# Performance work log

Hardware: AMD Instinct MI355X
Metric: run time of the kernel (lower is better)

Reference implementation:

```python
import jax, jax.numpy as jnp
import numpy as np

B, S, D = 4, 1024, 384
NUM_ITEMS = 16384
NUM_CLUSTERS = 256
MAX_CLUSTER_SIZE = 128  # 16384/256 = 64 real members, padded to 128 with -1
NEG_INF = -1e9


def setup_inputs() -> dict:
    key = jax.random.key(0)
    k1, k2, k3, k4, k5 = jax.random.split(key, 5)
    hidden_states = jax.random.normal(k1, (B, S, D), dtype=jnp.float32)
    item_embeddings = jax.random.normal(k2, (NUM_ITEMS, D), dtype=jnp.float32) * 0.02
    cluster_embeddings = jax.random.normal(k3, (NUM_CLUSTERS, D), dtype=jnp.float32) * 0.02
    targets = jax.random.randint(k4, (B, S), 0, NUM_ITEMS, dtype=jnp.int32)
    item_mask = (jax.random.uniform(k5, (B, S)) < 0.8).astype(jnp.float32)
    # Deterministic round-robin clustering: item i -> cluster i % C, slot i // C
    cluster_assignments = (jnp.arange(NUM_ITEMS, dtype=jnp.int32) % NUM_CLUSTERS)
    ids = (jnp.arange(NUM_CLUSTERS, dtype=jnp.int32)[:, None]
           + NUM_CLUSTERS * jnp.arange(MAX_CLUSTER_SIZE, dtype=jnp.int32)[None, :])
    cluster_indices = jnp.where(ids < NUM_ITEMS, ids, -1)  # [C, M], padded with -1
    in_cluster_id = (jnp.arange(NUM_ITEMS, dtype=jnp.int32) // NUM_CLUSTERS)
    return {
        "hidden_states": hidden_states,
        "item_embeddings": item_embeddings,
        "cluster_embeddings": cluster_embeddings,
        "item_mask": item_mask,
        "targets": targets,
        "cluster_assignments": cluster_assignments,
        "cluster_indices": cluster_indices,
        "in_cluster_id": in_cluster_id,
    }


def reference(hidden_states, item_embeddings, cluster_embeddings, item_mask,
              targets, cluster_assignments, cluster_indices, in_cluster_id):
    # Level 1: cluster logits / log-probs
    cluster_logits = jnp.einsum('bsd,cd->bsc', hidden_states, cluster_embeddings)
    cluster_log_probs = jax.nn.log_softmax(cluster_logits, axis=-1)
    target_cluster_ids = cluster_assignments[targets]                      # [B,S]
    target_cluster_log_prob = jnp.take_along_axis(
        cluster_log_probs, target_cluster_ids[..., None].astype(jnp.int32), axis=-1
    ).squeeze(-1)                                                          # [B,S]

    # Level 2: gather member embeddings of the target cluster, masked softmax
    cluster_members = cluster_indices[target_cluster_ids]                  # [B,S,M]
    member_emb = item_embeddings[jnp.maximum(cluster_members, 0)]          # [B,S,M,D]
    member_logits = jnp.einsum('bsd,bsmd->bsm', hidden_states, member_emb)  # [B,S,M]
    masked_logits = jnp.where(cluster_members != -1, member_logits, NEG_INF)
    member_log_probs = jax.nn.log_softmax(masked_logits, axis=-1)
    target_pos = in_cluster_id[targets]                                    # [B,S]
    target_item_log_prob = jnp.take_along_axis(
        member_log_probs, target_pos[..., None].astype(jnp.int32), axis=-1
    ).squeeze(-1)

    # Combined loss
    loss_per_token = -(target_cluster_log_prob + target_item_log_prob)
    total_loss = jnp.sum(loss_per_token * item_mask) / (jnp.sum(item_mask) + 1e-8)

    cluster_preds = jnp.argmax(cluster_logits, axis=-1)
    cluster_acc = jnp.mean((cluster_preds == target_cluster_ids).astype(jnp.float32))

    dummy_logits = jnp.zeros(hidden_states.shape[:2] + (item_embeddings.shape[0],),
                             dtype=hidden_states.dtype)
    return (dummy_logits, total_loss,
            -jnp.mean(target_cluster_log_prob),
            -jnp.mean(target_item_log_prob),
            cluster_acc)
```

## Files before the change

kernel.cpp:

```cpp
#include <hip/hip_runtime.h>
#include <math.h>

#define Ddim 384
#define D4 96
#define NUM_ITEMS 16384
#define NUM_CLUSTERS 256
#define NEG_INF_F (-1e9f)
#define NTOK 4096
#define TPB 16
#define NCB (NTOK / TPB)
#define NFB 512
#define FILL_F4 32768
#define RSTRIDE 97

__device__ __forceinline__ float dot4(const float4& a, const float4& b) {
    return a.x * b.x + a.y * b.y + a.z * b.z + a.w * b.w;
}
__device__ __forceinline__ void pin4(float4& v) {
    asm volatile("" : "+v"(v.x), "+v"(v.y), "+v"(v.z), "+v"(v.w));
}

__global__ __launch_bounds__(256, 2) void hs_mega(
    const float* __restrict__ hidden,
    const float* __restrict__ cluster_emb,
    const float* __restrict__ item_mask,
    const int*   __restrict__ targets,
    const int*   __restrict__ cluster_assign,
    float* __restrict__ dummy_out,
    float* __restrict__ ws,
    int*   __restrict__ wsI)
{
    const int bid = blockIdx.x;
    const int tid = threadIdx.x;

    __shared__ float4 ce_lds[32 * D4];
    __shared__ float  clog[TPB][NUM_CLUSTERS];
    __shared__ int    cnt[NUM_CLUSTERS];
    __shared__ int    scan[NUM_CLUSTERS];
    __shared__ int    cur[NUM_CLUSTERS];

    if (bid == NFB + NCB) {
        cnt[tid] = 0; cur[tid] = 0;
        __syncthreads();
        int tcv[NTOK / 256];
        #pragma unroll
        for (int i = 0; i < NTOK / 256; ++i) {
            const int t = i * 256 + tid;
            const int tc = cluster_assign[targets[t]];
            tcv[i] = tc;
            atomicAdd(&cnt[tc], 1);
        }
        __syncthreads();
        scan[tid] = cnt[tid];
        __syncthreads();
        for (int d = 1; d < 256; d <<= 1) {
            const int v = (tid >= d) ? scan[tid - d] : 0;
            __syncthreads();
            scan[tid] += v;
            __syncthreads();
        }
        wsI[tid] = scan[tid] - cnt[tid];
        if (tid == 255) wsI[256] = NTOK;
        __syncthreads();
        #pragma unroll
        for (int i = 0; i < NTOK / 256; ++i) {
            const int t = i * 256 + tid;
            const int tc = tcv[i];
            const int p = atomicAdd(&cur[tc], 1);
            wsI[257 + (scan[tc] - cnt[tc]) + p] = t;
        }
        return;
    }

    if (bid % 3 != 2) {
        const int fid = (bid / 3) * 2 + (bid % 3);
        float4 z; z.x = z.y = z.z = z.w = 0.f;
        float4* o4 = reinterpret_cast<float4*>(dummy_out)
                     + (size_t)fid * 256 + tid;
        #pragma unroll 8
        for (int i = 0; i < FILL_F4 / 256; ++i)
            o4[(size_t)i * (NFB * 256)] = z;
        return;
    }

    const int cb   = bid / 3;
    const int t0   = cb * TPB;
    const int lane = tid & 63;
    const int wid  = tid >> 6;
    const int q    = lane >> 4;
    const int r    = lane & 15;

    const int tw = t0 + wid * 4;
    const float4* h4 = reinterpret_cast<const float4*>(hidden);
    float4 hf[4][6];
    #pragma unroll
    for (int j = 0; j < 4; ++j)
        #pragma unroll
        for (int i = 0; i < 6; ++i) {
            hf[j][i] = h4[(size_t)(tw + j) * D4 + i * 16 + r];
            pin4(hf[j][i]);
        }

    const float4* ce4 = reinterpret_cast<const float4*>(cluster_emb);
    for (int ch = 0; ch < 8; ++ch) {
        __syncthreads();
        #pragma unroll
        for (int jj = 0; jj < 12; ++jj)
            ce_lds[jj * 256 + tid] = ce4[ch * 3072 + jj * 256 + tid];
        __syncthreads();

        #pragma unroll 2
        for (int it = 0; it < 8; ++it) {
            const int cl = it * 4 + q;
            float4 ce[6];
            #pragma unroll
            for (int i = 0; i < 6; ++i) ce[i] = ce_lds[cl * D4 + i * 16 + r];
            float a0 = 0.f, a1 = 0.f, a2 = 0.f, a3 = 0.f;
            #pragma unroll
            for (int i = 0; i < 6; ++i) {
                a0 += dot4(ce[i], hf[0][i]);
                a1 += dot4(ce[i], hf[1][i]);
                a2 += dot4(ce[i], hf[2][i]);
                a3 += dot4(ce[i], hf[3][i]);
            }
            const bool hi8 = (r & 8) != 0;
            float u  = hi8 ? a1 : a0;
            float uS = hi8 ? a0 : a1;
            u += __shfl_xor(uS, 8);
            float w  = hi8 ? a3 : a2;
            float wS = hi8 ? a2 : a3;
            w += __shfl_xor(wS, 8);
            const bool hi4 = (r & 4) != 0;
            float zv = hi4 ? w : u;
            float zS = hi4 ? u : w;
            zv += __shfl_xor(zS, 4);
            zv += __shfl_xor(zv, 2);
            zv += __shfl_xor(zv, 1);
            if ((r & 3) == 0) {
                const int m = (r >> 2) & 3;
                const int tokj = (m == 1) ? 2 : (m == 2) ? 1 : m;
                clog[wid * 4 + tokj][ch * 32 + cl] = zv;
            }
        }
    }
    __syncthreads();

    #pragma unroll
    for (int p = 0; p < 4; ++p) {
        const int t  = wid * 4 + p;
        const int gt = t0 + t;
        const float v0 = clog[t][lane];
        const float v1 = clog[t][lane + 64];
        const float v2 = clog[t][lane + 128];
        const float v3 = clog[t][lane + 192];
        float bv = v0; int bi = lane;
        if (v1 > bv) { bv = v1; bi = lane + 64;  }
        if (v2 > bv) { bv = v2; bi = lane + 128; }
        if (v3 > bv) { bv = v3; bi = lane + 192; }
        #pragma unroll
        for (int m = 32; m > 0; m >>= 1) {
            const float ov = __shfl_xor(bv, m);
            const int   oi = __shfl_xor(bi, m);
            if (ov > bv || (ov == bv && oi < bi)) { bv = ov; bi = oi; }
        }
        float e = expf(v0 - bv) + expf(v1 - bv) + expf(v2 - bv) + expf(v3 - bv);
        #pragma unroll
        for (int m = 32; m > 0; m >>= 1) e += __shfl_xor(e, m);
        const float lse = bv + logf(e);
        if (lane == 0) {
            const int tc = cluster_assign[targets[gt]];
            ws[NTOK + gt]     = item_mask[gt];
            ws[2 * NTOK + gt] = clog[t][tc] - lse;
            ws[4 * NTOK + gt] = (bi == tc) ? 1.f : 0.f;
        }
    }
}

__global__ __launch_bounds__(256) void hs_member(
    const float* __restrict__ hidden,
    const float* __restrict__ item_emb,
    const int*   __restrict__ targets,
    const int*   __restrict__ in_cluster_id,
    const int*   __restrict__ wsI,
    float* __restrict__ ws)
{
    const int c    = blockIdx.x;
    const int tid  = threadIdx.x;
    const int lane = tid & 63;
    const int wid  = tid >> 6;

    __shared__ float4 rows[64 * RSTRIDE];

    const int off  = wsI[c];
    const int cntc = wsI[c + 1] - off;
    if (cntc == 0) return;

    const float4* ie4 = reinterpret_cast<const float4*>(item_emb);
    for (int j = tid; j < 64 * D4; j += 256) {
        const int s = j / D4, col = j % D4;
        const int id = c + (s << 8);
        rows[s * RSTRIDE + (col ^ ((s >> 3) & 7))] = ie4[(size_t)id * D4 + col];
    }
    __syncthreads();

    const int  swz  = (lane >> 3) & 7;
    const int* list = wsI + 257;

    for (int i = wid * 2; i < cntc; i += 8) {
        const int tokA  = __builtin_amdgcn_readfirstlane(list[off + i]);
        const bool hasB = (i + 1) < cntc;
        const int tokB  = hasB ? __builtin_amdgcn_readfirstlane(list[off + i + 1]) : tokA;
        const float4* hA = reinterpret_cast<const float4*>(hidden + (size_t)tokA * Ddim);
        const float4* hB = reinterpret_cast<const float4*>(hidden + (size_t)tokB * Ddim);
        float mA = 0.f, mB = 0.f;
        #pragma unroll 8
        for (int k = 0; k < D4; ++k) {
            const float4 rv = rows[lane * RSTRIDE + (k ^ swz)];
            mA += dot4(rv, hA[k]);
            mB += dot4(rv, hB[k]);
        }
        float mxA = mA, mxB = mB;
        #pragma unroll
        for (int m = 32; m > 0; m >>= 1) {
            mxA = fmaxf(mxA, __shfl_xor(mxA, m));
            mxB = fmaxf(mxB, __shfl_xor(mxB, m));
        }
        float eA = expf(mA - mxA);
        float eB = expf(mB - mxB);
        #pragma unroll
        for (int m = 32; m > 0; m >>= 1) {
            eA += __shfl_xor(eA, m);
            eB += __shfl_xor(eB, m);
        }
        const int tpA = in_cluster_id[targets[tokA]];
        const int tpB = in_cluster_id[targets[tokB]];
        const float vA = __shfl(mA, tpA);
        const float vB = __shfl(mB, tpB);
        if (lane == 0) {
            ws[3 * NTOK + tokA] = vA - (mxA + logf(eA));
            if (hasB) ws[3 * NTOK + tokB] = vB - (mxB + logf(eB));
        }
    }
}

__global__ __launch_bounds__(1024) void hs_final(
    const float* __restrict__ ws, float* __restrict__ out)
{
    __shared__ double red[5][1024];
    const int tid = threadIdx.x;
    double a0 = 0, a1 = 0, a2 = 0, a3 = 0, a4 = 0;
    for (int i = tid; i < NTOK; i += 1024) {
        const float msk  = ws[NTOK + i];
        const float tlpc = ws[2 * NTOK + i];
        const float tlpi = ws[3 * NTOK + i];
        a0 += (double)(-(tlpc + tlpi) * msk);
        a1 += (double)msk;
        a2 += (double)tlpc;
        a3 += (double)tlpi;
        a4 += (double)ws[4 * NTOK + i];
    }
    red[0][tid] = a0; red[1][tid] = a1; red[2][tid] = a2;
    red[3][tid] = a3; red[4][tid] = a4;
    __syncthreads();
    for (int s2 = 512; s2 > 0; s2 >>= 1) {
        if (tid < s2) {
            red[0][tid] += red[0][tid + s2];
            red[1][tid] += red[1][tid + s2];
            red[2][tid] += red[2][tid + s2];
            red[3][tid] += red[3][tid + s2];
            red[4][tid] += red[4][tid + s2];
        }
        __syncthreads();
    }
    if (tid == 0) {
        out[0] = (float)(red[0][0] / (red[1][0] + 1e-8));
        out[1] = (float)(-red[2][0] / (double)NTOK);
        out[2] = (float)(-red[3][0] / (double)NTOK);
        out[3] = (float)(red[4][0] / (double)NTOK);
    }
}

extern "C" void kernel_launch(void* const* d_in, const int* in_sizes, int n_in,
                              void* d_out, int out_size, void* d_ws, size_t ws_size,
                              hipStream_t stream) {
    const float* hidden         = (const float*)d_in[0];
    const float* item_emb       = (const float*)d_in[1];
    const float* cluster_emb    = (const float*)d_in[2];
    const float* item_mask      = (const float*)d_in[3];
    const int*   targets        = (const int*)d_in[4];
    const int*   cluster_assign = (const int*)d_in[5];
    const int*   in_cluster_id  = (const int*)d_in[7];

    float* out = (float*)d_out;
    float* ws  = (float*)d_ws;
    int*   wsI = (int*)(ws + 5 * NTOK);

    const size_t dummy_elems = (size_t)NTOK * NUM_ITEMS;

    hs_mega<<<NFB + NCB + 1, 256, 0, stream>>>(
        hidden, cluster_emb, item_mask, targets, cluster_assign, out, ws, wsI);
    hs_member<<<NUM_CLUSTERS, 256, 0, stream>>>(
        hidden, item_emb, targets, in_cluster_id, wsI, ws);
    hs_final<<<1, 1024, 0, stream>>>(ws, out + dummy_elems);
}
```

Baseline: 128.5 us.

## Tile cluster-logit GEMM via LDS, stash logits in dummy output, split softmax

Replaces the per-token register-resident cluster-logit computation with a 64x64 tiled GEMM using double-buffered shared-memory staging and 4x4 register micro-tiles. The raw cluster logits are written temporarily into the first rows of the zero-filled dummy output. The log-softmax/argmax step moves into a second kernel that is interleaved with the member-level blocks, and a tail kernel re-zeroes that scratch region before the final reduction. The aim is to cut redundant loads of cluster embeddings and improve arithmetic reuse, at the cost of extra global round-trips for the logits and an additional zero-fill pass over part of the dummy output.

After: 142.1 us. +10.6%, slower.

```diff
diff --git a/kernel.cpp b/kernel.cpp
--- a/kernel.cpp
+++ b/kernel.cpp
@@ -7,39 +7,31 @@
 #define NUM_CLUSTERS 256
 #define NEG_INF_F (-1e9f)
 #define NTOK 4096
-#define TPB 16
-#define NCB (NTOK / TPB)
 #define NFB 512
-#define FILL_F4 32768
+#define NGB 256
 #define RSTRIDE 97
+#define KP 68
 
 __device__ __forceinline__ float dot4(const float4& a, const float4& b) {
     return a.x * b.x + a.y * b.y + a.z * b.z + a.w * b.w;
-}
-__device__ __forceinline__ void pin4(float4& v) {
-    asm volatile("" : "+v"(v.x), "+v"(v.y), "+v"(v.z), "+v"(v.w));
 }
 
 __global__ __launch_bounds__(256, 2) void hs_mega(
     const float* __restrict__ hidden,
     const float* __restrict__ cluster_emb,
-    const float* __restrict__ item_mask,
     const int*   __restrict__ targets,
     const int*   __restrict__ cluster_assign,
     float* __restrict__ dummy_out,
-    float* __restrict__ ws,
     int*   __restrict__ wsI)
 {
     const int bid = blockIdx.x;
     const int tid = threadIdx.x;
 
-    __shared__ float4 ce_lds[32 * D4];
-    __shared__ float  clog[TPB][NUM_CLUSTERS];
-    __shared__ int    cnt[NUM_CLUSTERS];
-    __shared__ int    scan[NUM_CLUSTERS];
-    __shared__ int    cur[NUM_CLUSTERS];
-
-    if (bid == NFB + NCB) {
+    __shared__ float hS[2][32][KP];
+    __shared__ float cS[2][32][KP];
+    __shared__ int   cnt[NUM_CLUSTERS], scan[NUM_CLUSTERS], cur[NUM_CLUSTERS];
+
+    if (bid == NFB + NGB) {
         cnt[tid] = 0; cur[tid] = 0;
         __syncthreads();
         int tcv[NTOK / 256];
@@ -75,122 +67,150 @@
     if (bid % 3 != 2) {
         const int fid = (bid / 3) * 2 + (bid % 3);
         float4 z; z.x = z.y = z.z = z.w = 0.f;
-        float4* o4 = reinterpret_cast<float4*>(dummy_out)
+        float4* o4 = reinterpret_cast<float4*>(dummy_out) + 262144
                      + (size_t)fid * 256 + tid;
-        #pragma unroll 8
-        for (int i = 0; i < FILL_F4 / 256; ++i)
+        #pragma unroll 7
+        for (int i = 0; i < 126; ++i)
             o4[(size_t)i * (NFB * 256)] = z;
         return;
     }
 
-    const int cb   = bid / 3;
-    const int t0   = cb * TPB;
-    const int lane = tid & 63;
-    const int wid  = tid >> 6;
-    const int q    = lane >> 4;
-    const int r    = lane & 15;
-
-    const int tw = t0 + wid * 4;
-    const float4* h4 = reinterpret_cast<const float4*>(hidden);
-    float4 hf[4][6];
+    const int g  = bid / 3;
+    const int t0 = (g & 63) * 64;
+    const int c0 = (g >> 6) * 64;
+    const int ty = tid >> 4;
+    const int tx = tid & 15;
+
+    const float4* hg = reinterpret_cast<const float4*>(hidden);
+    const float4* cg = reinterpret_cast<const float4*>(cluster_emb);
+
+    const int srow0 = tid >> 3, sc8 = tid & 7;
+
+    float acc[4][4];
     #pragma unroll
-    for (int j = 0; j < 4; ++j)
-        #pragma unroll
-        for (int i = 0; i < 6; ++i) {
-            hf[j][i] = h4[(size_t)(tw + j) * D4 + i * 16 + r];
-            pin4(hf[j][i]);
-        }
-
-    const float4* ce4 = reinterpret_cast<const float4*>(cluster_emb);
-    for (int ch = 0; ch < 8; ++ch) {
-        __syncthreads();
-        #pragma unroll
-        for (int jj = 0; jj < 12; ++jj)
-            ce_lds[jj * 256 + tid] = ce4[ch * 3072 + jj * 256 + tid];
-        __syncthreads();
-
-        #pragma unroll 2
-        for (int it = 0; it < 8; ++it) {
-            const int cl = it * 4 + q;
-            float4 ce[6];
+    for (int i = 0; i < 4; ++i)
+        #pragma unroll
+        for (int j = 0; j < 4; ++j) acc[i][j] = 0.f;
+
+    float4 rh[2], rc[2];
+    #pragma unroll
+    for (int ph = 0; ph < 2; ++ph) {
+        const int row = srow0 + ph * 32;
+        rh[ph] = hg[(size_t)(t0 + row) * D4 + sc8];
+        rc[ph] = cg[(size_t)(c0 + row) * D4 + sc8];
+    }
+    int cb = 0;
+    #pragma unroll
+    for (int ph = 0; ph < 2; ++ph) {
+        const int row = srow0 + ph * 32;
+        const int kl = sc8 * 4;
+        hS[0][kl+0][row] = rh[ph].x; hS[0][kl+1][row] = rh[ph].y;
+        hS[0][kl+2][row] = rh[ph].z; hS[0][kl+3][row] = rh[ph].w;
+        cS[0][kl+0][row] = rc[ph].x; cS[0][kl+1][row] = rc[ph].y;
+        cS[0][kl+2][row] = rc[ph].z; cS[0][kl+3][row] = rc[ph].w;
+    }
+    __syncthreads();
+
+    for (int kk = 0; kk < 12; ++kk) {
+        if (kk < 11) {
             #pragma unroll
-            for (int i = 0; i < 6; ++i) ce[i] = ce_lds[cl * D4 + i * 16 + r];
-            float a0 = 0.f, a1 = 0.f, a2 = 0.f, a3 = 0.f;
+            for (int ph = 0; ph < 2; ++ph) {
+                const int row = srow0 + ph * 32;
+                rh[ph] = hg[(size_t)(t0 + row) * D4 + (kk + 1) * 8 + sc8];
+                rc[ph] = cg[(size_t)(c0 + row) * D4 + (kk + 1) * 8 + sc8];
+            }
+        }
+        #pragma unroll
+        for (int k = 0; k < 32; ++k) {
+            const float4 hv = *reinterpret_cast<const float4*>(&hS[cb][k][ty * 4]);
+            const float4 cv = *reinterpret_cast<const float4*>(&cS[cb][k][tx * 4]);
+            acc[0][0] += hv.x * cv.x; acc[0][1] += hv.x * cv.y;
+            acc[0][2] += hv.x * cv.z; acc[0][3] += hv.x * cv.w;
+            acc[1][0] += hv.y * cv.x; acc[1][1] += hv.y * cv.y;
+            acc[1][2] += hv.y * cv.z; acc[1][3] += hv.y * cv.w;
+            acc[2][0] += hv.z * cv.x; acc[2][1] += hv.z * cv.y;
+            acc[2][2] += hv.z * cv.z; acc[2][3] += hv.z * cv.w;
+            acc[3][0] += hv.w * cv.x; acc[3][1] += hv.w * cv.y;
+            acc[3][2] += hv.w * cv.z; acc[3][3] += hv.w * cv.w;
+        }
+        if (kk < 11) {
+            const int nb = cb ^ 1;
             #pragma unroll
-            for (int i = 0; i < 6; ++i) {
-                a0 += dot4(ce[i], hf[0][i]);
-                a1 += dot4(ce[i], hf[1][i]);
-                a2 += dot4(ce[i], hf[2][i]);
-                a3 += dot4(ce[i], hf[3][i]);
+            for (int ph = 0; ph < 2; ++ph) {
+                const int row = srow0 + ph * 32;
+                const int kl = sc8 * 4;
+                hS[nb][kl+0][row] = rh[ph].x; hS[nb][kl+1][row] = rh[ph].y;
+                hS[nb][kl+2][row] = rh[ph].z; hS[nb][kl+3][row] = rh[ph].w;
+                cS[nb][kl+0][row] = rc[ph].x; cS[nb][kl+1][row] = rc[ph].y;
+                cS[nb][kl+2][row] = rc[ph].z; cS[nb][kl+3][row] = rc[ph].w;
             }
-            const bool hi8 = (r & 8) != 0;
-            float u  = hi8 ? a1 : a0;
-            float uS = hi8 ? a0 : a1;
-            u += __shfl_xor(uS, 8);
-            float w  = hi8 ? a3 : a2;
-            float wS = hi8 ? a2 : a3;
-            w += __shfl_xor(wS, 8);
-            const bool hi4 = (r & 4) != 0;
-            float zv = hi4 ? w : u;
-            float zS = hi4 ? u : w;
-            zv += __shfl_xor(zS, 4);
-            zv += __shfl_xor(zv, 2);
-            zv += __shfl_xor(zv, 1);
-            if ((r & 3) == 0) {
-                const int m = (r >> 2) & 3;
-                const int tokj = (m == 1) ? 2 : (m == 2) ? 1 : m;
-                clog[wid * 4 + tokj][ch * 32 + cl] = zv;
-            }
-        }
-    }
-    __syncthreads();
-
+            __syncthreads();
+            cb = nb;
+        }
+    }
+
+    float* clg = dummy_out;
     #pragma unroll
-    for (int p = 0; p < 4; ++p) {
-        const int t  = wid * 4 + p;
-        const int gt = t0 + t;
-        const float v0 = clog[t][lane];
-        const float v1 = clog[t][lane + 64];
-        const float v2 = clog[t][lane + 128];
-        const float v3 = clog[t][lane + 192];
-        float bv = v0; int bi = lane;
-        if (v1 > bv) { bv = v1; bi = lane + 64;  }
-        if (v2 > bv) { bv = v2; bi = lane + 128; }
-        if (v3 > bv) { bv = v3; bi = lane + 192; }
-        #pragma unroll
-        for (int m = 32; m > 0; m >>= 1) {
-            const float ov = __shfl_xor(bv, m);
-            const int   oi = __shfl_xor(bi, m);
-            if (ov > bv || (ov == bv && oi < bi)) { bv = ov; bi = oi; }
-        }
-        float e = expf(v0 - bv) + expf(v1 - bv) + expf(v2 - bv) + expf(v3 - bv);
-        #pragma unroll
-        for (int m = 32; m > 0; m >>= 1) e += __shfl_xor(e, m);
-        const float lse = bv + logf(e);
-        if (lane == 0) {
-            const int tc = cluster_assign[targets[gt]];
-            ws[NTOK + gt]     = item_mask[gt];
-            ws[2 * NTOK + gt] = clog[t][tc] - lse;
-            ws[4 * NTOK + gt] = (bi == tc) ? 1.f : 0.f;
-        }
-    }
-}
-
-__global__ __launch_bounds__(256) void hs_member(
+    for (int i = 0; i < 4; ++i) {
+        float4 v; v.x = acc[i][0]; v.y = acc[i][1]; v.z = acc[i][2]; v.w = acc[i][3];
+        *reinterpret_cast<float4*>(
+            &clg[(size_t)(t0 + ty * 4 + i) * NUM_CLUSTERS + c0 + tx * 4]) = v;
+    }
+}
+
+__global__ __launch_bounds__(256) void hs_phase2(
     const float* __restrict__ hidden,
     const float* __restrict__ item_emb,
+    const float* __restrict__ item_mask,
     const int*   __restrict__ targets,
+    const int*   __restrict__ cluster_assign,
     const int*   __restrict__ in_cluster_id,
+    const float* __restrict__ clg,
     const int*   __restrict__ wsI,
     float* __restrict__ ws)
 {
-    const int c    = blockIdx.x;
+    const int bid  = blockIdx.x;
     const int tid  = threadIdx.x;
     const int lane = tid & 63;
     const int wid  = tid >> 6;
 
     __shared__ float4 rows[64 * RSTRIDE];
 
+    if (bid & 1) {
+        const int t0 = (bid >> 1) * 16;
+        #pragma unroll
+        for (int p = 0; p < 4; ++p) {
+            const int gt = t0 + wid * 4 + p;
+            const float* row = clg + (size_t)gt * NUM_CLUSTERS;
+            const float v0 = row[lane];
+            const float v1 = row[lane + 64];
+            const float v2 = row[lane + 128];
+            const float v3 = row[lane + 192];
+            float bv = v0; int bi = lane;
+            if (v1 > bv) { bv = v1; bi = lane + 64;  }
+            if (v2 > bv) { bv = v2; bi = lane + 128; }
+            if (v3 > bv) { bv = v3; bi = lane + 192; }
+            #pragma unroll
+            for (int m = 32; m > 0; m >>= 1) {
+                const float ov = __shfl_xor(bv, m);
+                const int   oi = __shfl_xor(bi, m);
+                if (ov > bv || (ov == bv && oi < bi)) { bv = ov; bi = oi; }
+            }
+            float e = expf(v0 - bv) + expf(v1 - bv) + expf(v2 - bv) + expf(v3 - bv);
+            #pragma unroll
+            for (int m = 32; m > 0; m >>= 1) e += __shfl_xor(e, m);
+            const float lse = bv + logf(e);
+            if (lane == 0) {
+                const int tc = cluster_assign[targets[gt]];
+                ws[NTOK + gt]     = item_mask[gt];
+                ws[2 * NTOK + gt] = row[tc] - lse;
+                ws[4 * NTOK + gt] = (bi == tc) ? 1.f : 0.f;
+            }
+        }
+        return;
+    }
+
+    const int c    = bid >> 1;
     const int off  = wsI[c];
     const int cntc = wsI[c + 1] - off;
     if (cntc == 0) return;
@@ -243,13 +263,26 @@
     }
 }
 
-__global__ __launch_bounds__(1024) void hs_final(
-    const float* __restrict__ ws, float* __restrict__ out)
+__global__ __launch_bounds__(256) void hs_tail(
+    const float* __restrict__ ws, float* __restrict__ dummy_out,
+    float* __restrict__ out)
 {
-    __shared__ double red[5][1024];
+    const int bid = blockIdx.x;
     const int tid = threadIdx.x;
+
+    if (bid < 8) {
+        float4 z; z.x = z.y = z.z = z.w = 0.f;
+        float4* o4 = reinterpret_cast<float4*>(dummy_out)
+                     + (size_t)bid * 256 + tid;
+        #pragma unroll 8
+        for (int i = 0; i < 128; ++i)
+            o4[(size_t)i * 2048] = z;
+        return;
+    }
+
+    __shared__ double red[5][256];
     double a0 = 0, a1 = 0, a2 = 0, a3 = 0, a4 = 0;
-    for (int i = tid; i < NTOK; i += 1024) {
+    for (int i = tid; i < NTOK; i += 256) {
         const float msk  = ws[NTOK + i];
         const float tlpc = ws[2 * NTOK + i];
         const float tlpi = ws[3 * NTOK + i];
@@ -262,7 +295,7 @@
     red[0][tid] = a0; red[1][tid] = a1; red[2][tid] = a2;
     red[3][tid] = a3; red[4][tid] = a4;
     __syncthreads();
-    for (int s2 = 512; s2 > 0; s2 >>= 1) {
+    for (int s2 = 128; s2 > 0; s2 >>= 1) {
         if (tid < s2) {
             red[0][tid] += red[0][tid + s2];
             red[1][tid] += red[1][tid + s2];
@@ -297,9 +330,10 @@
 
     const size_t dummy_elems = (size_t)NTOK * NUM_ITEMS;
 
-    hs_mega<<<NFB + NCB + 1, 256, 0, stream>>>(
-        hidden, cluster_emb, item_mask, targets, cluster_assign, out, ws, wsI);
-    hs_member<<<NUM_CLUSTERS, 256, 0, stream>>>(
-        hidden, item_emb, targets, in_cluster_id, wsI, ws);
-    hs_final<<<1, 1024, 0, stream>>>(ws, out + dummy_elems);
-}
+    hs_mega<<<NFB + NGB + 1, 256, 0, stream>>>(
+        hidden, cluster_emb, targets, cluster_assign, out, wsI);
+    hs_phase2<<<2 * NUM_CLUSTERS, 256, 0, stream>>>(
+        hidden, item_emb, item_mask, targets, cluster_assign,
+        in_cluster_id, out, wsI, ws);
+    hs_tail<<<9, 256, 0, stream>>>(ws, out, out + dummy_elems);
+}
```

## Split mega kernel into separate fill/meta, member, and cluster kernels

Applied to the files above, without the earlier changes.

Breaks the combined kernel, which interleaved dummy-output zero-fill blocks with cluster-logit blocks, into a dedicated fill-plus-bucketing kernel with 2048 fill blocks, the member kernel, and a standalone cluster-logit kernel launched after it. The aim is to give the bandwidth-bound 256MB zero fill its own uniform grid and to stop compute blocks sharing CUs with store-heavy blocks. In exchange there is an extra kernel launch, and the cluster compute no longer overlaps the fill.

Result: slower. 150.5 us (+17.1%).

```diff
diff --git a/kernel.cpp b/kernel.cpp
--- a/kernel.cpp
+++ b/kernel.cpp
@@ -8,9 +8,7 @@
 #define NEG_INF_F (-1e9f)
 #define NTOK 4096
 #define TPB 16
-#define NCB (NTOK / TPB)
-#define NFB 512
-#define FILL_F4 32768
+#define NFILLB 2048
 #define RSTRIDE 97
 
 __device__ __forceinline__ float dot4(const float4& a, const float4& b) {
@@ -20,75 +18,139 @@
     asm volatile("" : "+v"(v.x), "+v"(v.y), "+v"(v.z), "+v"(v.w));
 }
 
-__global__ __launch_bounds__(256, 2) void hs_mega(
+__global__ __launch_bounds__(256) void hs_fill_meta(
+    const int* __restrict__ targets, const int* __restrict__ cluster_assign,
+    float* __restrict__ dummy_out, int* __restrict__ wsI)
+{
+    const int tid = threadIdx.x;
+
+    if (blockIdx.x == NFILLB) {
+        __shared__ int cnt[NUM_CLUSTERS], scan[NUM_CLUSTERS], cur[NUM_CLUSTERS];
+        cnt[tid] = 0; cur[tid] = 0;
+        __syncthreads();
+        int tcv[NTOK / 256];
+        #pragma unroll
+        for (int i = 0; i < NTOK / 256; ++i) {
+            const int t = i * 256 + tid;
+            const int tc = cluster_assign[targets[t]];
+            tcv[i] = tc;
+            atomicAdd(&cnt[tc], 1);
+        }
+        __syncthreads();
+        scan[tid] = cnt[tid];
+        __syncthreads();
+        for (int d = 1; d < 256; d <<= 1) {
+            const int v = (tid >= d) ? scan[tid - d] : 0;
+            __syncthreads();
+            scan[tid] += v;
+            __syncthreads();
+        }
+        wsI[tid] = scan[tid] - cnt[tid];
+        if (tid == 255) wsI[256] = NTOK;
+        __syncthreads();
+        #pragma unroll
+        for (int i = 0; i < NTOK / 256; ++i) {
+            const int t = i * 256 + tid;
+            const int tc = tcv[i];
+            const int p = atomicAdd(&cur[tc], 1);
+            wsI[257 + (scan[tc] - cnt[tc]) + p] = t;
+        }
+        return;
+    }
+
+    const size_t base = (size_t)blockIdx.x * 256 + tid;
+    float4 z; z.x = z.y = z.z = z.w = 0.f;
+    float4* o4 = reinterpret_cast<float4*>(dummy_out) + base;
+    #pragma unroll 8
+    for (int i = 0; i < 32; ++i)
+        o4[(size_t)i * (NFILLB * 256)] = z;
+}
+
+__global__ __launch_bounds__(256) void hs_member(
+    const float* __restrict__ hidden,
+    const float* __restrict__ item_emb,
+    const int*   __restrict__ targets,
+    const int*   __restrict__ in_cluster_id,
+    const int*   __restrict__ wsI,
+    float* __restrict__ ws)
+{
+    const int c    = blockIdx.x;
+    const int tid  = threadIdx.x;
+    const int lane = tid & 63;
+    const int wid  = tid >> 6;
+
+    __shared__ float4 rows[64 * RSTRIDE];
+
+    const int off  = wsI[c];
+    const int cntc = wsI[c + 1] - off;
+    if (cntc == 0) return;
+
+    const float4* ie4 = reinterpret_cast<const float4*>(item_emb);
+    for (int j = tid; j < 64 * D4; j += 256) {
+        const int s = j / D4, col = j % D4;
+        const int id = c + (s << 8);
+        rows[s * RSTRIDE + (col ^ ((s >> 3) & 7))] = ie4[(size_t)id * D4 + col];
+    }
+    __syncthreads();
+
+    const int  swz  = (lane >> 3) & 7;
+    const int* list = wsI + 257;
+
+    for (int i = wid * 2; i < cntc; i += 8) {
+        const int tokA  = __builtin_amdgcn_readfirstlane(list[off + i]);
+        const bool hasB = (i + 1) < cntc;
+        const int tokB  = hasB ? __builtin_amdgcn_readfirstlane(list[off + i + 1]) : tokA;
+        const float4* hA = reinterpret_cast<const float4*>(hidden + (size_t)tokA * Ddim);
+        const float4* hB = reinterpret_cast<const float4*>(hidden + (size_t)tokB * Ddim);
+        float mA = 0.f, mB = 0.f;
+        #pragma unroll 8
+        for (int k = 0; k < D4; ++k) {
+            const float4 rv = rows[lane * RSTRIDE + (k ^ swz)];
+            mA += dot4(rv, hA[k]);
+            mB += dot4(rv, hB[k]);
+        }
+        float mxA = mA, mxB = mB;
+        #pragma unroll
+        for (int m = 32; m > 0; m >>= 1) {
+            mxA = fmaxf(mxA, __shfl_xor(mxA, m));
+            mxB = fmaxf(mxB, __shfl_xor(mxB, m));
+        }
+        float eA = expf(mA - mxA);
+        float eB = expf(mB - mxB);
+        #pragma unroll
+        for (int m = 32; m > 0; m >>= 1) {
+            eA += __shfl_xor(eA, m);
+            eB += __shfl_xor(eB, m);
+        }
+        const int tpA = in_cluster_id[targets[tokA]];
+        const int tpB = in_cluster_id[targets[tokB]];
+        const float vA = __shfl(mA, tpA);
+        const float vB = __shfl(mB, tpB);
+        if (lane == 0) {
+            ws[3 * NTOK + tokA] = vA - (mxA + logf(eA));
+            if (hasB) ws[3 * NTOK + tokB] = vB - (mxB + logf(eB));
+        }
+    }
+}
+
+__global__ __launch_bounds__(256, 2) void hs_cluster(
     const float* __restrict__ hidden,
     const float* __restrict__ cluster_emb,
     const float* __restrict__ item_mask,
     const int*   __restrict__ targets,
     const int*   __restrict__ cluster_assign,
-    float* __restrict__ dummy_out,
-    float* __restrict__ ws,
-    int*   __restrict__ wsI)
+    float* __restrict__ ws)
 {
-    const int bid = blockIdx.x;
-    const int tid = threadIdx.x;
-
-    __shared__ float4 ce_lds[32 * D4];
-    __shared__ float  clog[TPB][NUM_CLUSTERS];
-    __shared__ int    cnt[NUM_CLUSTERS];
-    __shared__ int    scan[NUM_CLUSTERS];
-    __shared__ int    cur[NUM_CLUSTERS];
-
-    if (bid == NFB + NCB) {
-        cnt[tid] = 0; cur[tid] = 0;
-        __syncthreads();
-        int tcv[NTOK / 256];
-        #pragma unroll
-        for (int i = 0; i < NTOK / 256; ++i) {
-            const int t = i * 256 + tid;
-            const int tc = cluster_assign[targets[t]];
-            tcv[i] = tc;
-            atomicAdd(&cnt[tc], 1);
-        }
-        __syncthreads();
-        scan[tid] = cnt[tid];
-        __syncthreads();
-        for (int d = 1; d < 256; d <<= 1) {
-            const int v = (tid >= d) ? scan[tid - d] : 0;
-            __syncthreads();
-            scan[tid] += v;
-            __syncthreads();
-        }
-        wsI[tid] = scan[tid] - cnt[tid];
-        if (tid == 255) wsI[256] = NTOK;
-        __syncthreads();
-        #pragma unroll
-        for (int i = 0; i < NTOK / 256; ++i) {
-            const int t = i * 256 + tid;
-            const int tc = tcv[i];
-            const int p = atomicAdd(&cur[tc], 1);
-            wsI[257 + (scan[tc] - cnt[tc]) + p] = t;
-        }
-        return;
-    }
-
-    if (bid % 3 != 2) {
-        const int fid = (bid / 3) * 2 + (bid % 3);
-        float4 z; z.x = z.y = z.z = z.w = 0.f;
-        float4* o4 = reinterpret_cast<float4*>(dummy_out)
-                     + (size_t)fid * 256 + tid;
-        #pragma unroll 8
-        for (int i = 0; i < FILL_F4 / 256; ++i)
-            o4[(size_t)i * (NFB * 256)] = z;
-        return;
-    }
-
-    const int cb   = bid / 3;
+    const int cb   = blockIdx.x;
+    const int tid  = threadIdx.x;
     const int t0   = cb * TPB;
     const int lane = tid & 63;
     const int wid  = tid >> 6;
     const int q    = lane >> 4;
     const int r    = lane & 15;
+
+    __shared__ float4 ce_lds[32 * D4];
+    __shared__ float  clog[TPB][NUM_CLUSTERS];
 
     const int tw = t0 + wid * 4;
     const float4* h4 = reinterpret_cast<const float4*>(hidden);
@@ -176,73 +238,6 @@
     }
 }
 
-__global__ __launch_bounds__(256) void hs_member(
-    const float* __restrict__ hidden,
-    const float* __restrict__ item_emb,
-    const int*   __restrict__ targets,
-    const int*   __restrict__ in_cluster_id,
-    const int*   __restrict__ wsI,
-    float* __restrict__ ws)
-{
-    const int c    = blockIdx.x;
-    const int tid  = threadIdx.x;
-    const int lane = tid & 63;
-    const int wid  = tid >> 6;
-
-    __shared__ float4 rows[64 * RSTRIDE];
-
-    const int off  = wsI[c];
-    const int cntc = wsI[c + 1] - off;
-    if (cntc == 0) return;
-
-    const float4* ie4 = reinterpret_cast<const float4*>(item_emb);
-    for (int j = tid; j < 64 * D4; j += 256) {
-        const int s = j / D4, col = j % D4;
-        const int id = c + (s << 8);
-        rows[s * RSTRIDE + (col ^ ((s >> 3) & 7))] = ie4[(size_t)id * D4 + col];
-    }
-    __syncthreads();
-
-    const int  swz  = (lane >> 3) & 7;
-    const int* list = wsI + 257;
-
-    for (int i = wid * 2; i < cntc; i += 8) {
-        const int tokA  = __builtin_amdgcn_readfirstlane(list[off + i]);
-        const bool hasB = (i + 1) < cntc;
-        const int tokB  = hasB ? __builtin_amdgcn_readfirstlane(list[off + i + 1]) : tokA;
-        const float4* hA = reinterpret_cast<const float4*>(hidden + (size_t)tokA * Ddim);
-        const float4* hB = reinterpret_cast<const float4*>(hidden + (size_t)tokB * Ddim);
-        float mA = 0.f, mB = 0.f;
-        #pragma unroll 8
-        for (int k = 0; k < D4; ++k) {
-            const float4 rv = rows[lane * RSTRIDE + (k ^ swz)];
-            mA += dot4(rv, hA[k]);
-            mB += dot4(rv, hB[k]);
-        }
-        float mxA = mA, mxB = mB;
-        #pragma unroll
-        for (int m = 32; m > 0; m >>= 1) {
-            mxA = fmaxf(mxA, __shfl_xor(mxA, m));
-            mxB = fmaxf(mxB, __shfl_xor(mxB, m));
-        }
-        float eA = expf(mA - mxA);
-        float eB = expf(mB - mxB);
-        #pragma unroll
-        for (int m = 32; m > 0; m >>= 1) {
-            eA += __shfl_xor(eA, m);
-            eB += __shfl_xor(eB, m);
-        }
-        const int tpA = in_cluster_id[targets[tokA]];
-        const int tpB = in_cluster_id[targets[tokB]];
-        const float vA = __shfl(mA, tpA);
-        const float vB = __shfl(mB, tpB);
-        if (lane == 0) {
-            ws[3 * NTOK + tokA] = vA - (mxA + logf(eA));
-            if (hasB) ws[3 * NTOK + tokB] = vB - (mxB + logf(eB));
-        }
-    }
-}
-
 __global__ __launch_bounds__(1024) void hs_final(
     const float* __restrict__ ws, float* __restrict__ out)
 {
@@ -297,9 +292,11 @@
 
     const size_t dummy_elems = (size_t)NTOK * NUM_ITEMS;
 
-    hs_mega<<<NFB + NCB + 1, 256, 0, stream>>>(
-        hidden, cluster_emb, item_mask, targets, cluster_assign, out, ws, wsI);
+    hs_fill_meta<<<NFILLB + 1, 256, 0, stream>>>(
+        targets, cluster_assign, out, wsI);
     hs_member<<<NUM_CLUSTERS, 256, 0, stream>>>(
         hidden, item_emb, targets, in_cluster_id, wsI, ws);
+    hs_cluster<<<NUM_CLUSTERS, 256, 0, stream>>>(
+        hidden, cluster_emb, item_mask, targets, cluster_assign, ws);
     hs_final<<<1, 1024, 0, stream>>>(ws, out + dummy_elems);
 }
```
